# Kernel optimization log

Hardware: AMD Instinct MI355X
Metric: run time of the kernel (lower is better)

The kernel has to match this reference:

```python
import jax, jax.numpy as jnp
import numpy as np

B, N, C = 1, 2048, 1024
H, D = 16, 64          # num_heads, head_dim
S = 8                  # number of frames; tokens per frame = N // S
NEG_INF = jnp.float32(-1e30)  # stand-in for -inf, numerically safe under jit


def setup_inputs() -> dict:
    key = jax.random.key(0)
    ks = jax.random.split(key, 8)
    x = jax.random.normal(ks[0], (B, N, C), dtype=jnp.float32)
    # tokens grouped contiguously by frame (sorted frame ids)
    frame_ids = jnp.repeat(jnp.arange(S, dtype=jnp.int32), N // S)
    is_hub = jax.random.bernoulli(ks[1], 0.05, (N,))
    adj = jax.random.bernoulli(ks[2], 0.25, (S, S))
    adj = adj.at[jnp.arange(S), jnp.arange(S)].set(True)  # frames always see self
    frame_bias = jax.random.normal(ks[3], (S, S), dtype=jnp.float32) * 0.1
    Wqkv = jax.random.normal(ks[4], (C, 3 * C), dtype=jnp.float32) * 0.02
    bqkv = jnp.zeros((3 * C,), dtype=jnp.float32)
    Wproj = jax.random.normal(ks[5], (C, C), dtype=jnp.float32) * 0.02
    bproj = jnp.zeros((C,), dtype=jnp.float32)
    return {"x": x, "frame_ids": frame_ids, "is_hub": is_hub, "adj": adj,
            "frame_bias": frame_bias, "Wqkv": Wqkv, "bqkv": bqkv,
            "Wproj": Wproj, "bproj": bproj}


def reference(x, frame_ids, is_hub, adj, frame_bias, Wqkv, bqkv, Wproj, bproj):
    # qkv projection: (B,N,3C) -> (3,B,H,N,D)
    qkv = (x @ Wqkv + bqkv).reshape(B, N, 3, H, D).transpose(2, 0, 3, 1, 4)
    q, k, v = qkv[0], qkv[1], qkv[2]

    # flex_attention: scores scaled by 1/sqrt(D) BEFORE score_mod
    scores = jnp.einsum("bhnd,bhmd->bhnm", q, k) * (D ** -0.5)

    # score_mod, vectorized over all (qi,kj) pairs:
    fi = frame_ids                                   # (N,)
    allow = adj[fi][:, fi]                           # (N,N) frame adjacency per token pair
    diff_frame = fi[:, None] != fi[None, :]
    hub_block = diff_frame & (is_hub[:, None] | is_hub[None, :])
    allow = allow & ~hub_block                       # mask_hub_tokens=True
    bias = frame_bias[fi][:, fi]                     # soft_mask=True: add frame-level bias

    scores = jnp.where(allow, scores + bias, NEG_INF)  # broadcast over (b,h)
    attn = jax.nn.softmax(scores, axis=-1)
    out = jnp.einsum("bhnm,bhmd->bhnd", attn, v)
    out = out.transpose(0, 2, 1, 3).reshape(B, N, C)
    return out @ Wproj + bproj
```

## Files before the change

kernel.cpp:

```cpp
#include <hip/hip_runtime.h>

#define NTOK 2048
#define CDIM 1024
#define NHEAD 16
#define HDIM 64
#define NFRM 8
#define FTOK 256

typedef unsigned short ushort;
typedef unsigned long long u64;
typedef __attribute__((ext_vector_type(8))) short short8;
typedef __attribute__((ext_vector_type(8))) ushort ushort8;
typedef __attribute__((ext_vector_type(4))) ushort ushort4v;
typedef __attribute__((ext_vector_type(4))) float floatx4;

__device__ __forceinline__ ushort f2bf(float f) {
    unsigned int u = __float_as_uint(f);
    return (ushort)((u + 0x7fffu + ((u >> 16) & 1u)) >> 16);
}

__device__ __forceinline__ void gload_lds16(const void* g, void* l) {
    __builtin_amdgcn_global_load_lds(
        (const __attribute__((address_space(1))) unsigned int*)(uintptr_t)g,
        (__attribute__((address_space(3))) unsigned int*)(unsigned int)(uintptr_t)l,
        16, 0, 0);
}

__global__ __launch_bounds__(256)
void prep_kernel(const float* __restrict__ x, ushort* __restrict__ xb,
                 const float* __restrict__ Wqkv, ushort* __restrict__ wqkvT,
                 const float* __restrict__ Wproj, ushort* __restrict__ wprojT,
                 const int* __restrict__ is_hub, u64* __restrict__ hubmask)
{
    __shared__ ushort LT[64][72];
    const int b = blockIdx.x, t = threadIdx.x;

    if (b < 2048) {
        int i = b * 256 + t;
        float4 f = ((const float4*)x)[i];
        ushort4v o = { f2bf(f.x), f2bf(f.y), f2bf(f.z), f2bf(f.w) };
        ((ushort4v*)xb)[i] = o;
        return;
    }
    if (b >= 3072) {
        if (t < NTOK / 64) {
            u64 m = 0;
            for (int j = 0; j < 64; ++j)
                m |= (u64)(is_hub[t * 64 + j] != 0) << j;
            hubmask[t] = m;
        }
        return;
    }

    const float* W; ushort* WT; int K, N, n0, k0;
    if (b < 2816) { int idx = b - 2048; W = Wqkv;  WT = wqkvT;  K = 1024; N = 3072;
                    n0 = (idx % 48) * 64; k0 = (idx / 48) * 64; }
    else          { int idx = b - 2816; W = Wproj; WT = wprojT; K = 1024; N = 1024;
                    n0 = (idx & 15) * 64; k0 = (idx >> 4) * 64; }

    const int kr = t >> 4, nc = t & 15;
#pragma unroll
    for (int i = 0; i < 4; ++i) {
        int k = kr + i * 16;
        float4 w4 = *(const float4*)(W + (size_t)(k0 + k) * N + n0 + nc * 4);
        LT[nc*4+0][k] = f2bf(w4.x);
        LT[nc*4+1][k] = f2bf(w4.y);
        LT[nc*4+2][k] = f2bf(w4.z);
        LT[nc*4+3][k] = f2bf(w4.w);
    }
    __syncthreads();
    const int n = t >> 2;
#pragma unroll
    for (int half = 0; half < 2; ++half) {
        int kc = (t & 3) + 4 * half;
        ushort8 v = *(const ushort8*)&LT[n][kc * 8];
        *(ushort8*)(WT + (size_t)(n0 + n) * K + k0 + kc * 8) = v;
    }
}

__global__ __launch_bounds__(256)
void vtrans_kernel(const ushort* __restrict__ v, ushort* __restrict__ vT)
{
    __shared__ ushort LT[64][72];
    const int t = threadIdx.x, h = blockIdx.y, n0 = blockIdx.x * 64;
    {
        const int tok = t >> 2;
#pragma unroll
        for (int half = 0; half < 2; ++half) {
            int dc = (t & 3) + 4 * half;
            ushort8 v8 = *(const ushort8*)(v + ((size_t)h * NTOK + n0 + tok) * HDIM + dc * 8);
#pragma unroll
            for (int j = 0; j < 8; ++j) LT[dc*8 + j][tok] = v8[j];
        }
    }
    __syncthreads();
    {
        const int d = t >> 2;
#pragma unroll
        for (int half = 0; half < 2; ++half) {
            int tc = (t & 3) + 4 * half;
            ushort8 o8 = *(const ushort8*)&LT[d][tc * 8];
            *(ushort8*)(vT + ((size_t)h * HDIM + d) * NTOK + n0 + tc * 8) = o8;
        }
    }
}

__global__ __launch_bounds__(256)
void gemm_bt_kernel(const ushort* __restrict__ A, const ushort* __restrict__ BT,
                    const float* __restrict__ bias, void* __restrict__ out,
                    int M, int N, int K, int mode)
{
    __shared__ ushort As[2][128 * 32];
    __shared__ ushort Bs[2][128 * 32];

    const int t = threadIdx.x;
    const int wave = t >> 6, lane = t & 63;
    const int quad = lane >> 4, l15 = lane & 15;
    const int row0 = blockIdx.y * 128, col0 = blockIdx.x * 128;
    const int wm = (wave >> 1) * 64, wn = (wave & 1) * 64;

    const int sr = lane >> 2;
    const int sc = (lane & 3) * 8;
    const int r0 = wave * 32;

    floatx4 acc[4][4];
#pragma unroll
    for (int i = 0; i < 4; ++i)
#pragma unroll
        for (int j = 0; j < 4; ++j) acc[i][j] = (floatx4){0.f, 0.f, 0.f, 0.f};

    gload_lds16(A  + (size_t)(row0 + r0      + sr) * K + sc, &As[0][ r0       * 32]);
    gload_lds16(A  + (size_t)(row0 + r0 + 16 + sr) * K + sc, &As[0][(r0 + 16) * 32]);
    gload_lds16(BT + (size_t)(col0 + r0      + sr) * K + sc, &Bs[0][ r0       * 32]);
    gload_lds16(BT + (size_t)(col0 + r0 + 16 + sr) * K + sc, &Bs[0][(r0 + 16) * 32]);

    const int nk = K >> 5;
    for (int ki = 0; ki < nk; ++ki) {
        __syncthreads();
        if (ki + 1 < nk) {
            const int kn = (ki + 1) << 5;
            const int b = (ki + 1) & 1;
            gload_lds16(A  + (size_t)(row0 + r0      + sr) * K + kn + sc, &As[b][ r0       * 32]);
            gload_lds16(A  + (size_t)(row0 + r0 + 16 + sr) * K + kn + sc, &As[b][(r0 + 16) * 32]);
            gload_lds16(BT + (size_t)(col0 + r0      + sr) * K + kn + sc, &Bs[b][ r0       * 32]);
            gload_lds16(BT + (size_t)(col0 + r0 + 16 + sr) * K + kn + sc, &Bs[b][(r0 + 16) * 32]);
        }
        const ushort* as = As[ki & 1];
        const ushort* bs = Bs[ki & 1];

        short8 af[4], bfr[4];
#pragma unroll
        for (int i = 0; i < 4; ++i)
            af[i] = *(const short8*)&as[(wm + i * 16 + l15) * 32 + quad * 8];
#pragma unroll
        for (int j = 0; j < 4; ++j)
            bfr[j] = *(const short8*)&bs[(wn + j * 16 + l15) * 32 + quad * 8];
#pragma unroll
        for (int i = 0; i < 4; ++i)
#pragma unroll
            for (int j = 0; j < 4; ++j)
                acc[i][j] = __builtin_amdgcn_mfma_f32_16x16x32_bf16(af[i], bfr[j], acc[i][j], 0, 0, 0);
    }

    if (mode == 0) {
        float* outf = (float*)out;
#pragma unroll
        for (int j = 0; j < 4; ++j) {
            int col = col0 + wn + j * 16 + l15;
            float bb = bias[col];
#pragma unroll
            for (int i = 0; i < 4; ++i) {
                int rowb = row0 + wm + i * 16 + quad * 4;
#pragma unroll
                for (int r = 0; r < 4; ++r)
                    outf[(size_t)(rowb + r) * N + col] = acc[i][j][r] + bb;
            }
        }
    } else {
        ushort* outb = (ushort*)out;
#pragma unroll
        for (int j = 0; j < 4; ++j) {
            int col = col0 + wn + j * 16 + l15;
            float bb = bias[col];
            int part = col >> 10, hh = (col >> 6) & 15, d = col & 63;
            ushort* dst = outb + ((size_t)(part * NHEAD + hh) * NTOK) * HDIM + d;
#pragma unroll
            for (int i = 0; i < 4; ++i) {
                int rowb = row0 + wm + i * 16 + quad * 4;
#pragma unroll
                for (int r = 0; r < 4; ++r)
                    dst[(size_t)(rowb + r) * HDIM] = f2bf(acc[i][j][r] + bb);
            }
        }
    }
}

__global__ __launch_bounds__(256)
void attn_split_kernel(const ushort* __restrict__ qkvb,
                       const ushort* __restrict__ vTb,
                       const int* __restrict__ frame_ids,
                       const u64* __restrict__ hubmask,
                       const int* __restrict__ adj,
                       const float* __restrict__ frame_bias,
                       ushort* __restrict__ attnb)
{
    __shared__ float SH[4 * 16 * 68 + 64];
    ushort* PsAll = (ushort*)SH;

    const int t = threadIdx.x;
    const int wave = t >> 6, lane = t & 63;
    const int quad = lane >> 4, l15 = lane & 15;
    const int b = blockIdx.x;
    const int h = b & 15, q0 = (b >> 4) * 16;

    const ushort* Qg = qkvb + ((size_t)h * NTOK) * HDIM;
    const ushort* Kg = qkvb + ((size_t)(NHEAD + h) * NTOK) * HDIM;
    const ushort* Vg = vTb + ((size_t)h * HDIM) * NTOK;
    ushort* Ps = PsAll + wave * (16 * 72);

    short8 aq0 = *(const short8*)(Qg + (size_t)(q0 + l15) * HDIM + quad * 8);
    short8 aq1 = *(const short8*)(Qg + (size_t)(q0 + l15) * HDIM + 32 + quad * 8);

    const int fq = frame_ids[q0];
    unsigned vpack = 0; int nv = 0;
#pragma unroll
    for (int f = 0; f < NFRM; ++f)
        if (adj[fq * NFRM + f]) { vpack |= (unsigned)f << (3 * nv); ++nv; }

    const u64 hmq = hubmask[q0 >> 6] >> (q0 & 63);
    int qh[4];
#pragma unroll
    for (int r = 0; r < 4; ++r) qh[r] = (int)((hmq >> (quad * 4 + r)) & 1);

    float lpart[4] = {0.f, 0.f, 0.f, 0.f};
    floatx4 oacc[4];
#pragma unroll
    for (int dt = 0; dt < 4; ++dt) oacc[dt] = (floatx4){0.f, 0.f, 0.f, 0.f};

    for (int i = 0; i < nv; ++i) {
        const int fj = (int)((vpack >> (3 * i)) & 7u);
        const int k0 = fj * FTOK + wave * 64;
        const float fb = frame_bias[fq * NFRM + fj];
        const bool same = (fj == fq);
        const u64 hmk = hubmask[k0 >> 6];

        floatx4 s[4];
#pragma unroll
        for (int nt = 0; nt < 4; ++nt) {
            const ushort* kp = Kg + (size_t)(k0 + nt * 16 + l15) * HDIM;
            short8 bk0 = *(const short8*)(kp + quad * 8);
            short8 bk1 = *(const short8*)(kp + 32 + quad * 8);
            s[nt] = (floatx4){0.f, 0.f, 0.f, 0.f};
            s[nt] = __builtin_amdgcn_mfma_f32_16x16x32_bf16(aq0, bk0, s[nt], 0, 0, 0);
            s[nt] = __builtin_amdgcn_mfma_f32_16x16x32_bf16(aq1, bk1, s[nt], 0, 0, 0);
        }

        int kh[4];
#pragma unroll
        for (int nt = 0; nt < 4; ++nt) kh[nt] = (int)((hmk >> (nt * 16 + l15)) & 1);

#pragma unroll
        for (int r = 0; r < 4; ++r) {
            float ps = 0.f;
#pragma unroll
            for (int nt = 0; nt < 4; ++nt) {
                bool allow = same || ((qh[r] == 0) && (kh[nt] == 0));
                float sv = allow ? fmaf(s[nt][r], 0.125f, fb) : -1.0e30f;
                float p = __expf(sv);
                ps += p;
                Ps[(quad * 4 + r) * 72 + nt * 16 + l15] = f2bf(p);
            }
            lpart[r] += ps;
        }

        short8 ap0 = *(const short8*)&Ps[l15 * 72 + quad * 8];
        short8 ap1 = *(const short8*)&Ps[l15 * 72 + 32 + quad * 8];
#pragma unroll
        for (int dt = 0; dt < 4; ++dt) {
            const ushort* vp = Vg + (size_t)(dt * 16 + l15) * NTOK + k0;
            short8 bv0 = *(const short8*)(vp + quad * 8);
            short8 bv1 = *(const short8*)(vp + 32 + quad * 8);
            oacc[dt] = __builtin_amdgcn_mfma_f32_16x16x32_bf16(ap0, bv0, oacc[dt], 0, 0, 0);
            oacc[dt] = __builtin_amdgcn_mfma_f32_16x16x32_bf16(ap1, bv1, oacc[dt], 0, 0, 0);
        }
    }

#pragma unroll
    for (int r = 0; r < 4; ++r) {
        float ls = lpart[r];
        ls += __shfl_xor(ls, 1);
        ls += __shfl_xor(ls, 2);
        ls += __shfl_xor(ls, 4);
        ls += __shfl_xor(ls, 8);
        lpart[r] = ls;
    }

    __syncthreads();

#pragma unroll
    for (int dt = 0; dt < 4; ++dt)
#pragma unroll
        for (int r = 0; r < 4; ++r)
            SH[(wave * 16 + quad * 4 + r) * 68 + dt * 16 + l15] = oacc[dt][r];
    if (l15 == 0)
#pragma unroll
        for (int r = 0; r < 4; ++r)
            SH[4 * 16 * 68 + wave * 16 + quad * 4 + r] = lpart[r];

    __syncthreads();

    {
        const int row = t >> 4, cg = (t & 15) * 4;
        float4 o = {0.f, 0.f, 0.f, 0.f};
        float l = 0.f;
#pragma unroll
        for (int w = 0; w < 4; ++w) {
            float4 ow = *(const float4*)&SH[(w * 16 + row) * 68 + cg];
            o.x += ow.x; o.y += ow.y; o.z += ow.z; o.w += ow.w;
            l += SH[4 * 16 * 68 + w * 16 + row];
        }
        float li = 1.0f / l;
        ushort4v ob = { f2bf(o.x * li), f2bf(o.y * li), f2bf(o.z * li), f2bf(o.w * li) };
        *(ushort4v*)(attnb + (size_t)(q0 + row) * CDIM + h * HDIM + cg) = ob;
    }
}

extern "C" void kernel_launch(void* const* d_in, const int* in_sizes, int n_in,
                              void* d_out, int out_size, void* d_ws, size_t ws_size,
                              hipStream_t stream)
{
    const float* x          = (const float*)d_in[0];
    const int*   frame_ids  = (const int*)d_in[1];
    const int*   is_hub     = (const int*)d_in[2];
    const int*   adj        = (const int*)d_in[3];
    const float* frame_bias = (const float*)d_in[4];
    const float* Wqkv       = (const float*)d_in[5];
    const float* bqkv       = (const float*)d_in[6];
    const float* Wproj      = (const float*)d_in[7];
    const float* bproj      = (const float*)d_in[8];
    float* out = (float*)d_out;

    ushort* xb     = (ushort*)d_ws;
    ushort* wqkvT  = xb     + 2097152;
    ushort* wprojT = wqkvT  + 3145728;
    ushort* qkvb   = wprojT + 1048576;
    ushort* vTb    = qkvb   + 6291456;
    ushort* attnb  = vTb    + 2097152;
    u64*    hubmask = (u64*)(attnb + 2097152);

    prep_kernel<<<dim3(3073), dim3(256), 0, stream>>>(
        x, xb, Wqkv, wqkvT, Wproj, wprojT, is_hub, hubmask);

    gemm_bt_kernel<<<dim3(3 * CDIM / 128, NTOK / 128), dim3(256), 0, stream>>>(
        xb, wqkvT, bqkv, qkvb, NTOK, 3 * CDIM, CDIM, 1);

    vtrans_kernel<<<dim3(NTOK / 64, NHEAD), dim3(256), 0, stream>>>(
        qkvb + (size_t)2 * NHEAD * NTOK * HDIM, vTb);

    attn_split_kernel<<<dim3(2048), dim3(256), 0, stream>>>(
        qkvb, vTb, frame_ids, hubmask, adj, frame_bias, attnb);

    gemm_bt_kernel<<<dim3(CDIM / 128, NTOK / 128), dim3(256), 0, stream>>>(
        attnb, wprojT, bproj, out, NTOK, CDIM, CDIM, 0);
}
```

Before: 173.4 us.

## Fuse V transpose into QKV GEMM epilogue and use single-wave attention blocks

After: 183.1 us. 1.06x slower.

```diff
diff --git a/kernel.cpp b/kernel.cpp
--- a/kernel.cpp
+++ b/kernel.cpp
@@ -79,35 +79,9 @@
 }
 
 __global__ __launch_bounds__(256)
-void vtrans_kernel(const ushort* __restrict__ v, ushort* __restrict__ vT)
-{
-    __shared__ ushort LT[64][72];
-    const int t = threadIdx.x, h = blockIdx.y, n0 = blockIdx.x * 64;
-    {
-        const int tok = t >> 2;
-#pragma unroll
-        for (int half = 0; half < 2; ++half) {
-            int dc = (t & 3) + 4 * half;
-            ushort8 v8 = *(const ushort8*)(v + ((size_t)h * NTOK + n0 + tok) * HDIM + dc * 8);
-#pragma unroll
-            for (int j = 0; j < 8; ++j) LT[dc*8 + j][tok] = v8[j];
-        }
-    }
-    __syncthreads();
-    {
-        const int d = t >> 2;
-#pragma unroll
-        for (int half = 0; half < 2; ++half) {
-            int tc = (t & 3) + 4 * half;
-            ushort8 o8 = *(const ushort8*)&LT[d][tc * 8];
-            *(ushort8*)(vT + ((size_t)h * HDIM + d) * NTOK + n0 + tc * 8) = o8;
-        }
-    }
-}
-
-__global__ __launch_bounds__(256)
 void gemm_bt_kernel(const ushort* __restrict__ A, const ushort* __restrict__ BT,
                     const float* __restrict__ bias, void* __restrict__ out,
+                    ushort* __restrict__ vtb,
                     int M, int N, int K, int mode)
 {
     __shared__ ushort As[2][128 * 32];
@@ -183,32 +157,41 @@
             int col = col0 + wn + j * 16 + l15;
             float bb = bias[col];
             int part = col >> 10, hh = (col >> 6) & 15, d = col & 63;
-            ushort* dst = outb + ((size_t)(part * NHEAD + hh) * NTOK) * HDIM + d;
-#pragma unroll
-            for (int i = 0; i < 4; ++i) {
-                int rowb = row0 + wm + i * 16 + quad * 4;
-#pragma unroll
-                for (int r = 0; r < 4; ++r)
-                    dst[(size_t)(rowb + r) * HDIM] = f2bf(acc[i][j][r] + bb);
-            }
-        }
-    }
-}
-
-__global__ __launch_bounds__(256)
-void attn_split_kernel(const ushort* __restrict__ qkvb,
-                       const ushort* __restrict__ vTb,
-                       const int* __restrict__ frame_ids,
-                       const u64* __restrict__ hubmask,
-                       const int* __restrict__ adj,
-                       const float* __restrict__ frame_bias,
-                       ushort* __restrict__ attnb)
+            if (part < 2) {
+                ushort* dst = outb + ((size_t)(part * NHEAD + hh) * NTOK) * HDIM + d;
+#pragma unroll
+                for (int i = 0; i < 4; ++i) {
+                    int rowb = row0 + wm + i * 16 + quad * 4;
+#pragma unroll
+                    for (int r = 0; r < 4; ++r)
+                        dst[(size_t)(rowb + r) * HDIM] = f2bf(acc[i][j][r] + bb);
+                }
+            } else {
+                ushort* dst = vtb + ((size_t)hh * HDIM + d) * NTOK;
+#pragma unroll
+                for (int i = 0; i < 4; ++i) {
+                    int rowb = row0 + wm + i * 16 + quad * 4;
+#pragma unroll
+                    for (int r = 0; r < 4; ++r)
+                        dst[rowb + r] = f2bf(acc[i][j][r] + bb);
+                }
+            }
+        }
+    }
+}
+
+__global__ __launch_bounds__(64)
+void attn_wave_kernel(const ushort* __restrict__ qkvb,
+                      const ushort* __restrict__ vTb,
+                      const int* __restrict__ frame_ids,
+                      const u64* __restrict__ hubmask,
+                      const int* __restrict__ adj,
+                      const float* __restrict__ frame_bias,
+                      ushort* __restrict__ attnb)
 {
-    __shared__ float SH[4 * 16 * 68 + 64];
-    ushort* PsAll = (ushort*)SH;
-
-    const int t = threadIdx.x;
-    const int wave = t >> 6, lane = t & 63;
+    __shared__ ushort Ps[16 * 144];
+
+    const int lane = threadIdx.x;
     const int quad = lane >> 4, l15 = lane & 15;
     const int b = blockIdx.x;
     const int h = b & 15, q0 = (b >> 4) * 16;
@@ -216,7 +199,6 @@
     const ushort* Qg = qkvb + ((size_t)h * NTOK) * HDIM;
     const ushort* Kg = qkvb + ((size_t)(NHEAD + h) * NTOK) * HDIM;
     const ushort* Vg = vTb + ((size_t)h * HDIM) * NTOK;
-    ushort* Ps = PsAll + wave * (16 * 72);
 
     short8 aq0 = *(const short8*)(Qg + (size_t)(q0 + l15) * HDIM + quad * 8);
     short8 aq1 = *(const short8*)(Qg + (size_t)(q0 + l15) * HDIM + 32 + quad * 8);
@@ -226,6 +208,7 @@
 #pragma unroll
     for (int f = 0; f < NFRM; ++f)
         if (adj[fq * NFRM + f]) { vpack |= (unsigned)f << (3 * nv); ++nv; }
+    const int ntot2 = nv * 2;
 
     const u64 hmq = hubmask[q0 >> 6] >> (q0 & 63);
     int qh[4];
@@ -237,54 +220,87 @@
 #pragma unroll
     for (int dt = 0; dt < 4; ++dt) oacc[dt] = (floatx4){0.f, 0.f, 0.f, 0.f};
 
-    for (int i = 0; i < nv; ++i) {
-        const int fj = (int)((vpack >> (3 * i)) & 7u);
-        const int k0 = fj * FTOK + wave * 64;
+    auto blk_k0 = [&](int it) -> int {
+        const int fj = (int)((vpack >> (3 * (it >> 1))) & 7u);
+        return fj * FTOK + (it & 1) * 128;
+    };
+
+    auto load_k = [&](int k0, short8 (&ka)[2][4], short8 (&kb)[2][4]) {
+#pragma unroll
+        for (int tt = 0; tt < 2; ++tt)
+#pragma unroll
+            for (int nt = 0; nt < 4; ++nt) {
+                const ushort* kp = Kg + (size_t)(k0 + tt * 64 + nt * 16 + l15) * HDIM;
+                ka[tt][nt] = *(const short8*)(kp + quad * 8);
+                kb[tt][nt] = *(const short8*)(kp + 32 + quad * 8);
+            }
+    };
+
+    auto do_iter = [&](int it,
+                       short8 (&kaC)[2][4], short8 (&kbC)[2][4],
+                       short8 (&kaN)[2][4], short8 (&kbN)[2][4]) {
+        const int fj = (int)((vpack >> (3 * (it >> 1))) & 7u);
+        const int k0 = fj * FTOK + (it & 1) * 128;
         const float fb = frame_bias[fq * NFRM + fj];
         const bool same = (fj == fq);
-        const u64 hmk = hubmask[k0 >> 6];
-
-        floatx4 s[4];
-#pragma unroll
-        for (int nt = 0; nt < 4; ++nt) {
-            const ushort* kp = Kg + (size_t)(k0 + nt * 16 + l15) * HDIM;
-            short8 bk0 = *(const short8*)(kp + quad * 8);
-            short8 bk1 = *(const short8*)(kp + 32 + quad * 8);
-            s[nt] = (floatx4){0.f, 0.f, 0.f, 0.f};
-            s[nt] = __builtin_amdgcn_mfma_f32_16x16x32_bf16(aq0, bk0, s[nt], 0, 0, 0);
-            s[nt] = __builtin_amdgcn_mfma_f32_16x16x32_bf16(aq1, bk1, s[nt], 0, 0, 0);
-        }
-
-        int kh[4];
-#pragma unroll
-        for (int nt = 0; nt < 4; ++nt) kh[nt] = (int)((hmk >> (nt * 16 + l15)) & 1);
+        const u64 hm0 = hubmask[k0 >> 6];
+        const u64 hm1 = hubmask[(k0 >> 6) + 1];
+
+        floatx4 s[2][4];
+#pragma unroll
+        for (int tt = 0; tt < 2; ++tt)
+#pragma unroll
+            for (int nt = 0; nt < 4; ++nt) {
+                s[tt][nt] = (floatx4){0.f, 0.f, 0.f, 0.f};
+                s[tt][nt] = __builtin_amdgcn_mfma_f32_16x16x32_bf16(aq0, kaC[tt][nt], s[tt][nt], 0, 0, 0);
+                s[tt][nt] = __builtin_amdgcn_mfma_f32_16x16x32_bf16(aq1, kbC[tt][nt], s[tt][nt], 0, 0, 0);
+            }
+
+        if (it + 1 < ntot2) load_k(blk_k0(it + 1), kaN, kbN);
 
 #pragma unroll
         for (int r = 0; r < 4; ++r) {
             float ps = 0.f;
 #pragma unroll
-            for (int nt = 0; nt < 4; ++nt) {
-                bool allow = same || ((qh[r] == 0) && (kh[nt] == 0));
-                float sv = allow ? fmaf(s[nt][r], 0.125f, fb) : -1.0e30f;
-                float p = __expf(sv);
-                ps += p;
-                Ps[(quad * 4 + r) * 72 + nt * 16 + l15] = f2bf(p);
+            for (int tt = 0; tt < 2; ++tt) {
+                const u64 hm = tt ? hm1 : hm0;
+#pragma unroll
+                for (int nt = 0; nt < 4; ++nt) {
+                    int kh = (int)((hm >> (nt * 16 + l15)) & 1);
+                    bool allow = same || ((qh[r] == 0) && (kh == 0));
+                    float sv = allow ? fmaf(s[tt][nt][r], 0.125f, fb) : -1.0e30f;
+                    float p = __expf(sv);
+                    ps += p;
+                    Ps[(quad * 4 + r) * 144 + tt * 72 + nt * 16 + l15] = f2bf(p);
+                }
             }
             lpart[r] += ps;
         }
 
-        short8 ap0 = *(const short8*)&Ps[l15 * 72 + quad * 8];
-        short8 ap1 = *(const short8*)&Ps[l15 * 72 + 32 + quad * 8];
-#pragma unroll
-        for (int dt = 0; dt < 4; ++dt) {
-            const ushort* vp = Vg + (size_t)(dt * 16 + l15) * NTOK + k0;
-            short8 bv0 = *(const short8*)(vp + quad * 8);
-            short8 bv1 = *(const short8*)(vp + 32 + quad * 8);
-            oacc[dt] = __builtin_amdgcn_mfma_f32_16x16x32_bf16(ap0, bv0, oacc[dt], 0, 0, 0);
-            oacc[dt] = __builtin_amdgcn_mfma_f32_16x16x32_bf16(ap1, bv1, oacc[dt], 0, 0, 0);
-        }
-    }
-
+#pragma unroll
+        for (int tt = 0; tt < 2; ++tt) {
+            short8 ap0 = *(const short8*)&Ps[l15 * 144 + tt * 72 + quad * 8];
+            short8 ap1 = *(const short8*)&Ps[l15 * 144 + tt * 72 + 32 + quad * 8];
+#pragma unroll
+            for (int dt = 0; dt < 4; ++dt) {
+                const ushort* vp = Vg + (size_t)(dt * 16 + l15) * NTOK + k0 + tt * 64;
+                short8 bv0 = *(const short8*)(vp + quad * 8);
+                short8 bv1 = *(const short8*)(vp + 32 + quad * 8);
+                oacc[dt] = __builtin_amdgcn_mfma_f32_16x16x32_bf16(ap0, bv0, oacc[dt], 0, 0, 0);
+                oacc[dt] = __builtin_amdgcn_mfma_f32_16x16x32_bf16(ap1, bv1, oacc[dt], 0, 0, 0);
+            }
+        }
+    };
+
+    short8 kaA[2][4], kbA[2][4], kaB[2][4], kbB[2][4];
+    load_k(blk_k0(0), kaA, kbA);
+
+    for (int it = 0; it < ntot2; it += 2) {
+        do_iter(it,     kaA, kbA, kaB, kbB);
+        do_iter(it + 1, kaB, kbB, kaA, kbA);
+    }
+
+    float linv[4];
 #pragma unroll
     for (int r = 0; r < 4; ++r) {
         float ls = lpart[r];
@@ -292,36 +308,17 @@
         ls += __shfl_xor(ls, 2);
         ls += __shfl_xor(ls, 4);
         ls += __shfl_xor(ls, 8);
-        lpart[r] = ls;
-    }
-
-    __syncthreads();
-
-#pragma unroll
-    for (int dt = 0; dt < 4; ++dt)
-#pragma unroll
-        for (int r = 0; r < 4; ++r)
-            SH[(wave * 16 + quad * 4 + r) * 68 + dt * 16 + l15] = oacc[dt][r];
-    if (l15 == 0)
-#pragma unroll
-        for (int r = 0; r < 4; ++r)
-            SH[4 * 16 * 68 + wave * 16 + quad * 4 + r] = lpart[r];
-
-    __syncthreads();
-
-    {
-        const int row = t >> 4, cg = (t & 15) * 4;
-        float4 o = {0.f, 0.f, 0.f, 0.f};
-        float l = 0.f;
-#pragma unroll
-        for (int w = 0; w < 4; ++w) {
-            float4 ow = *(const float4*)&SH[(w * 16 + row) * 68 + cg];
-            o.x += ow.x; o.y += ow.y; o.z += ow.z; o.w += ow.w;
-            l += SH[4 * 16 * 68 + w * 16 + row];
-        }
-        float li = 1.0f / l;
-        ushort4v ob = { f2bf(o.x * li), f2bf(o.y * li), f2bf(o.z * li), f2bf(o.w * li) };
-        *(ushort4v*)(attnb + (size_t)(q0 + row) * CDIM + h * HDIM + cg) = ob;
+        linv[r] = 1.0f / ls;
+    }
+
+#pragma unroll
+    for (int dt = 0; dt < 4; ++dt) {
+        int col = h * HDIM + dt * 16 + l15;
+#pragma unroll
+        for (int r = 0; r < 4; ++r) {
+            int row = q0 + quad * 4 + r;
+            attnb[(size_t)row * CDIM + col] = f2bf(oacc[dt][r] * linv[r]);
+        }
     }
 }
 
@@ -352,14 +349,11 @@
         x, xb, Wqkv, wqkvT, Wproj, wprojT, is_hub, hubmask);
 
     gemm_bt_kernel<<<dim3(3 * CDIM / 128, NTOK / 128), dim3(256), 0, stream>>>(
-        xb, wqkvT, bqkv, qkvb, NTOK, 3 * CDIM, CDIM, 1);
-
-    vtrans_kernel<<<dim3(NTOK / 64, NHEAD), dim3(256), 0, stream>>>(
-        qkvb + (size_t)2 * NHEAD * NTOK * HDIM, vTb);
-
-    attn_split_kernel<<<dim3(2048), dim3(256), 0, stream>>>(
+        xb, wqkvT, bqkv, qkvb, vTb, NTOK, 3 * CDIM, CDIM, 1);
+
+    attn_wave_kernel<<<dim3(2048), dim3(64), 0, stream>>>(
         qkvb, vTb, frame_ids, hubmask, adj, frame_bias, attnb);
 
     gemm_bt_kernel<<<dim3(CDIM / 128, NTOK / 128), dim3(256), 0, stream>>>(
-        attnb, wprojT, bproj, out, NTOK, CDIM, CDIM, 0);
-}
+        attnb, wprojT, bproj, out, nullptr, NTOK, CDIM, CDIM, 0);
+}
```
